# Performance work log

Measured on AMD Instinct MI355X. Metric: run time of the kernel, lower is better.

## Reference

```python
import jax, jax.numpy as jnp
import numpy as np

N = 50000
E = 800000
IN_CH = 128
HID = 32
HEADS = 8
OUT_CH = 64
NEG_SLOPE = 0.2  # PyG GATConv default leaky_relu slope


def setup_inputs() -> dict:
    key = jax.random.key(0)
    ks = jax.random.split(key, 16)
    x = jax.random.normal(ks[0], (N, IN_CH), dtype=jnp.float32)
    edge_index = jax.random.randint(ks[1], (2, E), 0, N, dtype=jnp.int64)
    s = 0.1
    return {
        "x": x,
        "edge_index": edge_index,
        # layer 1: in -> (HEADS, HID), concat
        "W1": jax.random.normal(ks[2], (IN_CH, HEADS * HID), dtype=jnp.float32) * s,
        "att_src1": jax.random.normal(ks[3], (HEADS, HID), dtype=jnp.float32) * s,
        "att_dst1": jax.random.normal(ks[4], (HEADS, HID), dtype=jnp.float32) * s,
        "b1": jnp.zeros((HEADS * HID,), dtype=jnp.float32),
        # layer 2: HEADS*HID -> (HEADS, HID), concat
        "W2": jax.random.normal(ks[5], (HEADS * HID, HEADS * HID), dtype=jnp.float32) * s,
        "att_src2": jax.random.normal(ks[6], (HEADS, HID), dtype=jnp.float32) * s,
        "att_dst2": jax.random.normal(ks[7], (HEADS, HID), dtype=jnp.float32) * s,
        "b2": jnp.zeros((HEADS * HID,), dtype=jnp.float32),
        # layer 3: HEADS*HID -> (1, OUT_CH), no concat (heads=1)
        "W3": jax.random.normal(ks[8], (HEADS * HID, OUT_CH), dtype=jnp.float32) * s,
        "att_src3": jax.random.normal(ks[9], (1, OUT_CH), dtype=jnp.float32) * s,
        "att_dst3": jax.random.normal(ks[10], (1, OUT_CH), dtype=jnp.float32) * s,
        "b3": jnp.zeros((OUT_CH,), dtype=jnp.float32),
    }


def gat_conv(x, src, dst, W, a_src, a_dst, b, heads, ch, concat):
    n = x.shape[0]
    h = (x @ W).reshape(n, heads, ch)                      # [N,H,C]
    alpha_src = jnp.sum(h * a_src, axis=-1)                # [N,H]
    alpha_dst = jnp.sum(h * a_dst, axis=-1)                # [N,H]
    logits = jax.nn.leaky_relu(alpha_src[src] + alpha_dst[dst], NEG_SLOPE)  # [E,H]
    # numerically stable softmax over edges grouped by destination node
    m = jax.ops.segment_max(logits, dst, num_segments=n)   # [N,H]
    m = jnp.where(jnp.isfinite(m), m, 0.0)
    e = jnp.exp(logits - m[dst])                           # [E,H]
    denom = jax.ops.segment_sum(e, dst, num_segments=n)    # [N,H]
    alpha = e / (denom[dst] + 1e-16)                       # [E,H]
    # weighted scatter-aggregate of source features
    out = jax.ops.segment_sum(alpha[:, :, None] * h[src], dst, num_segments=n)  # [N,H,C]
    out = out.reshape(n, heads * ch) if concat else out.mean(axis=1)
    return out + b


def reference(x, edge_index, W1, att_src1, att_dst1, b1,
              W2, att_src2, att_dst2, b2, W3, att_src3, att_dst3, b3):
    src, dst = edge_index[0], edge_index[1]
    h = jax.nn.elu(gat_conv(x, src, dst, W1, att_src1, att_dst1, b1, HEADS, HID, True))
    h = jax.nn.elu(gat_conv(h, src, dst, W2, att_src2, att_dst2, b2, HEADS, HID, True))
    out = gat_conv(h, src, dst, W3, att_src3, att_dst3, b3, 1, OUT_CH, False)
    return out
```

## Files before the change

kernel.cpp:

```cpp
#include <hip/hip_runtime.h>
#include <hip/hip_bf16.h>
#include <hip/hip_fp16.h>
#include <stdint.h>

#define NNODES 50000
#define NEDGES 800000

typedef float f32x4 __attribute__((ext_vector_type(4)));
typedef _Float16 half8 __attribute__((ext_vector_type(8)));

__device__ __forceinline__ ushort f2h(float f) {
  return __half_as_ushort(__float2half(f));
}
__device__ __forceinline__ float2 h2x2(uint32_t u) {
  return __half22float2(__builtin_bit_cast(__half2, u));
}

__device__ __forceinline__ void gload_lds16(const void* g, void* l) {
  __builtin_amdgcn_global_load_lds(
      (const __attribute__((address_space(1))) uint32_t*)g,
      (__attribute__((address_space(3))) uint32_t*)l, 16, 0, 0);
}

__global__ __launch_bounds__(256) void gemm_wide(
    const ushort* __restrict__ A, const ushort* __restrict__ B,
    const float* __restrict__ a_src, const float* __restrict__ a_dst,
    float* __restrict__ as_out, float* __restrict__ ad_out,
    ushort* __restrict__ Cout, int M, int K) {
  __shared__ ushort As[64 * 64];
  __shared__ ushort Bs[256 * 64];

  const int t = threadIdx.x;
  const int w = t >> 6, ln = t & 63;
  const int row0 = blockIdx.x * 64;
  const int wr = (w >> 1) * 32, wc = (w & 1) * 128;

  f32x4 acc[2][8] = {};

  const int nkt = K >> 6;
  for (int kt = 0; kt < nkt; ++kt) {
    const int k0 = kt << 6;
    #pragma unroll
    for (int i = 0; i < 2; ++i) {
      int row8 = w * 2 + i;
      int rloc = row8 * 8 + (ln >> 3);
      int slot = (ln & 7) ^ (rloc & 7);
      int grow = row0 + rloc; grow = grow < M ? grow : M - 1;
      gload_lds16(A + (size_t)grow * K + k0 + slot * 8, As + row8 * 512);
    }
    #pragma unroll
    for (int i = 0; i < 8; ++i) {
      int row8 = w * 8 + i;
      int rloc = row8 * 8 + (ln >> 3);
      int slot = (ln & 7) ^ (rloc & 7);
      gload_lds16(B + (size_t)rloc * K + k0 + slot * 8, Bs + row8 * 512);
    }
    __syncthreads();

    #pragma unroll
    for (int ks = 0; ks < 2; ++ks) {
      half8 a[2], b[8];
      #pragma unroll
      for (int i = 0; i < 2; ++i) {
        int row = wr + i * 16 + (ln & 15);
        int slot = (ks * 4 + (ln >> 4)) ^ (row & 7);
        a[i] = *(const half8*)(As + row * 64 + slot * 8);
      }
      #pragma unroll
      for (int j = 0; j < 8; ++j) {
        int col = wc + j * 16 + (ln & 15);
        int slot = (ks * 4 + (ln >> 4)) ^ (col & 7);
        b[j] = *(const half8*)(Bs + col * 64 + slot * 8);
      }
      #pragma unroll
      for (int i = 0; i < 2; ++i)
        #pragma unroll
        for (int j = 0; j < 8; ++j)
          acc[i][j] = __builtin_amdgcn_mfma_f32_16x16x32_f16(a[i], b[j], acc[i][j], 0, 0, 0);
    }
    __syncthreads();
  }

  const int lx = ln & 15, g = ln >> 4;

  #pragma unroll
  for (int i = 0; i < 2; ++i)
    #pragma unroll
    for (int j = 0; j < 8; ++j)
      #pragma unroll
      for (int r = 0; r < 4; ++r) {
        int grow = row0 + wr + i * 16 + g * 4 + r;
        int gcol = wc + j * 16 + lx;
        if (grow < M) Cout[(size_t)grow * 256 + gcol] = f2h(acc[i][j][r]);
      }

  const int hbase = wc >> 5;
  float avs[8], avd[8];
  #pragma unroll
  for (int j = 0; j < 8; ++j) {
    avs[j] = a_src[wc + j * 16 + lx];
    avd[j] = a_dst[wc + j * 16 + lx];
  }
  #pragma unroll
  for (int i = 0; i < 2; ++i)
    #pragma unroll
    for (int r = 0; r < 4; ++r) {
      float ps[4] = {0.f, 0.f, 0.f, 0.f}, pd[4] = {0.f, 0.f, 0.f, 0.f};
      #pragma unroll
      for (int j = 0; j < 8; ++j) {
        float v = acc[i][j][r];
        ps[j >> 1] += v * avs[j];
        pd[j >> 1] += v * avd[j];
      }
      #pragma unroll
      for (int m = 1; m < 16; m <<= 1)
        #pragma unroll
        for (int q = 0; q < 4; ++q) {
          ps[q] += __shfl_xor(ps[q], m);
          pd[q] += __shfl_xor(pd[q], m);
        }
      if (lx == 0) {
        int grow = row0 + wr + i * 16 + g * 4 + r;
        if (grow < M) {
          #pragma unroll
          for (int q = 0; q < 4; ++q) {
            as_out[grow * 8 + hbase + q] = ps[q];
            ad_out[grow * 8 + hbase + q] = pd[q];
          }
        }
      }
    }
}

__global__ __launch_bounds__(256) void gemm_mfma3(
    const ushort* __restrict__ A, const ushort* __restrict__ B,
    const float* __restrict__ a_src, const float* __restrict__ a_dst,
    float* __restrict__ as_out, float* __restrict__ ad_out,
    ushort* __restrict__ Cout, int M, int K, int Ncols) {
  __shared__ ushort As[128 * 64];
  __shared__ ushort Bs[64 * 64];
  __shared__ float redS[2][128], redD[2][128];

  const int t = threadIdx.x;
  const int w = t >> 6, ln = t & 63;
  const int row0 = blockIdx.y * 128;
  const int col0 = blockIdx.x * 64;
  const int wr = (w >> 1) * 64, wc = (w & 1) * 32;

  f32x4 acc[4][2] = {};

  const int nkt = K >> 6;
  for (int kt = 0; kt < nkt; ++kt) {
    const int k0 = kt << 6;
    #pragma unroll
    for (int i = 0; i < 4; ++i) {
      int row8 = w * 4 + i;
      int rloc = row8 * 8 + (ln >> 3);
      int slot = (ln & 7) ^ (rloc & 7);
      int grow = row0 + rloc; grow = grow < M ? grow : M - 1;
      gload_lds16(A + (size_t)grow * K + k0 + slot * 8, As + row8 * 512);
    }
    #pragma unroll
    for (int i = 0; i < 2; ++i) {
      int row8 = w * 2 + i;
      int rloc = row8 * 8 + (ln >> 3);
      int slot = (ln & 7) ^ (rloc & 7);
      gload_lds16(B + (size_t)(col0 + rloc) * K + k0 + slot * 8, Bs + row8 * 512);
    }
    __syncthreads();

    #pragma unroll
    for (int ks = 0; ks < 2; ++ks) {
      half8 a[4], b[2];
      #pragma unroll
      for (int i = 0; i < 4; ++i) {
        int row = wr + i * 16 + (ln & 15);
        int slot = (ks * 4 + (ln >> 4)) ^ (row & 7);
        a[i] = *(const half8*)(As + row * 64 + slot * 8);
      }
      #pragma unroll
      for (int j = 0; j < 2; ++j) {
        int col = wc + j * 16 + (ln & 15);
        int slot = (ks * 4 + (ln >> 4)) ^ (col & 7);
        b[j] = *(const half8*)(Bs + col * 64 + slot * 8);
      }
      #pragma unroll
      for (int i = 0; i < 4; ++i)
        #pragma unroll
        for (int j = 0; j < 2; ++j)
          acc[i][j] = __builtin_amdgcn_mfma_f32_16x16x32_f16(a[i], b[j], acc[i][j], 0, 0, 0);
    }
    __syncthreads();
  }

  const int lx = ln & 15, g = ln >> 4;

  #pragma unroll
  for (int i = 0; i < 4; ++i)
    #pragma unroll
    for (int j = 0; j < 2; ++j)
      #pragma unroll
      for (int r = 0; r < 4; ++r) {
        int grow = row0 + wr + i * 16 + g * 4 + r;
        int gcol = col0 + wc + j * 16 + lx;
        if (grow < M) Cout[(size_t)grow * Ncols + gcol] = f2h(acc[i][j][r]);
      }

  float avs[2], avd[2];
  #pragma unroll
  for (int j = 0; j < 2; ++j) {
    avs[j] = a_src[wc + j * 16 + lx];
    avd[j] = a_dst[wc + j * 16 + lx];
  }
  #pragma unroll
  for (int i = 0; i < 4; ++i)
    #pragma unroll
    for (int r = 0; r < 4; ++r) {
      float ps = 0.f, pd = 0.f;
      #pragma unroll
      for (int j = 0; j < 2; ++j) {
        float v = acc[i][j][r];
        ps += v * avs[j];
        pd += v * avd[j];
      }
      #pragma unroll
      for (int m = 1; m < 16; m <<= 1) {
        ps += __shfl_xor(ps, m);
        pd += __shfl_xor(pd, m);
      }
      if (lx == 0) {
        int lrow = wr + i * 16 + g * 4 + r;
        redS[w & 1][lrow] = ps;
        redD[w & 1][lrow] = pd;
      }
    }
  __syncthreads();
  if (t < 128) {
    int grow = row0 + t;
    if (grow < M) {
      as_out[grow] = redS[0][t] + redS[1][t];
      ad_out[grow] = redD[0][t] + redD[1][t];
    }
  }
}

__global__ void cvt_h(const float* __restrict__ in, ushort* __restrict__ out, int n4) {
  int idx = blockIdx.x * blockDim.x + threadIdx.x;
  if (idx >= n4) return;
  float4 v = ((const float4*)in)[idx];
  ushort4 o;
  o.x = f2h(v.x); o.y = f2h(v.y); o.z = f2h(v.z); o.w = f2h(v.w);
  ((ushort4*)out)[idx] = o;
}

__global__ void cvt_w(const float* __restrict__ W, ushort* __restrict__ tr,
                      int K, int N) {
  int idx = blockIdx.x * blockDim.x + threadIdx.x;
  if (idx >= K * N) return;
  int k = idx / N, c = idx - k * N;
  tr[(size_t)c * K + k] = f2h(W[idx]);
}

__global__ void deg_kernel(const int* __restrict__ dst, int* __restrict__ deg, int E) {
  int e = blockIdx.x * blockDim.x + threadIdx.x;
  if (e < E) atomicAdd(&deg[dst[e]], 1);
}

__global__ __launch_bounds__(256) void scan_partial(const int* __restrict__ deg,
                                                    int* __restrict__ rowptr,
                                                    int* __restrict__ blocksum, int n) {
  __shared__ int sdata[256];
  int t = threadIdx.x;
  int base = blockIdx.x * 1024 + t * 4;
  int v[4], s = 0;
  #pragma unroll
  for (int i = 0; i < 4; ++i) {
    v[i] = (base + i < n) ? deg[base + i] : 0;
    s += v[i];
  }
  sdata[t] = s;
  __syncthreads();
  for (int off = 1; off < 256; off <<= 1) {
    int x = (t >= off) ? sdata[t - off] : 0;
    __syncthreads();
    sdata[t] += x;
    __syncthreads();
  }
  int run = sdata[t] - s;
  #pragma unroll
  for (int i = 0; i < 4; ++i) {
    if (base + i < n) rowptr[base + i] = run;
    run += v[i];
  }
  if (t == 255) blocksum[blockIdx.x] = sdata[255];
}

__global__ __launch_bounds__(256) void scan_blocksums(int* __restrict__ blocksum, int nb) {
  __shared__ int sdata[256];
  int t = threadIdx.x;
  int v = (t < nb) ? blocksum[t] : 0;
  sdata[t] = v;
  __syncthreads();
  for (int off = 1; off < 256; off <<= 1) {
    int x = (t >= off) ? sdata[t - off] : 0;
    __syncthreads();
    sdata[t] += x;
    __syncthreads();
  }
  if (t < nb) blocksum[t] = sdata[t] - v;
}

__global__ void scan_add(int* __restrict__ rowptr, const int* __restrict__ blocksum,
                         int* __restrict__ cursor, int n, int E) {
  int idx = blockIdx.x * blockDim.x + threadIdx.x;
  if (idx < n) {
    rowptr[idx] += blocksum[idx >> 10];
    cursor[idx] = 0;
  }
  if (idx == n) rowptr[n] = E;
}

__global__ void scatter_kernel(const int* __restrict__ src, const int* __restrict__ dst,
                               const int* __restrict__ rowptr, int* __restrict__ cursor,
                               int* __restrict__ col_src, int E) {
  int e = blockIdx.x * blockDim.x + threadIdx.x;
  if (e >= E) return;
  int d = dst[e];
  int pos = rowptr[d] + atomicAdd(&cursor[d], 1);
  col_src[pos] = src[e];
}

__global__ __launch_bounds__(256) void aggr_h(
    const int* __restrict__ rowptr, const int* __restrict__ col_src,
    const ushort* __restrict__ h, const float* __restrict__ as_,
    const float* __restrict__ ad_, const float* __restrict__ bias,
    ushort* __restrict__ of, int n) {
  int d = blockIdx.x * 4 + (threadIdx.x >> 6);
  if (d >= n) return;
  int lane = threadIdx.x & 63;
  int c0 = lane * 4;
  int hd = lane >> 3;
  float ad_d = ad_[d * 8 + hd];
  float a0 = 0.f, a1 = 0.f, a2 = 0.f, a3 = 0.f, denom = 0.f;
  int beg = rowptr[d], end = rowptr[d + 1];
  int i = beg;
  for (; i + 2 <= end; i += 2) {
    int s0 = col_src[i], s1 = col_src[i + 1];
    float l0 = as_[s0 * 8 + hd] + ad_d;
    float l1 = as_[s1 * 8 + hd] + ad_d;
    uint2 v0 = *(const uint2*)(h + (size_t)s0 * 256 + c0);
    uint2 v1 = *(const uint2*)(h + (size_t)s1 * 256 + c0);
    l0 = (l0 > 0.f) ? l0 : 0.2f * l0;
    l1 = (l1 > 0.f) ? l1 : 0.2f * l1;
    float e0 = __expf(l0), e1 = __expf(l1);
    denom += e0 + e1;
    float2 p0 = h2x2(v0.x), p1 = h2x2(v0.y);
    float2 q0 = h2x2(v1.x), q1 = h2x2(v1.y);
    a0 += e0 * p0.x + e1 * q0.x;
    a1 += e0 * p0.y + e1 * q0.y;
    a2 += e0 * p1.x + e1 * q1.x;
    a3 += e0 * p1.y + e1 * q1.y;
  }
  if (i < end) {
    int s = col_src[i];
    float l = as_[s * 8 + hd] + ad_d;
    l = (l > 0.f) ? l : 0.2f * l;
    float ev = __expf(l);
    denom += ev;
    uint2 v = *(const uint2*)(h + (size_t)s * 256 + c0);
    float2 p0 = h2x2(v.x), p1 = h2x2(v.y);
    a0 += ev * p0.x;
    a1 += ev * p0.y;
    a2 += ev * p1.x;
    a3 += ev * p1.y;
  }
  float inv = 1.f / (denom + 1e-16f);
  float v0 = a0 * inv + bias[c0 + 0];
  float v1 = a1 * inv + bias[c0 + 1];
  float v2 = a2 * inv + bias[c0 + 2];
  float v3 = a3 * inv + bias[c0 + 3];
  v0 = (v0 > 0.f) ? v0 : expm1f(v0);
  v1 = (v1 > 0.f) ? v1 : expm1f(v1);
  v2 = (v2 > 0.f) ? v2 : expm1f(v2);
  v3 = (v3 > 0.f) ? v3 : expm1f(v3);
  ushort4 hh;
  hh.x = f2h(v0); hh.y = f2h(v1); hh.z = f2h(v2); hh.w = f2h(v3);
  *(ushort4*)(of + (size_t)d * 256 + c0) = hh;
}

__global__ __launch_bounds__(256) void aggr_f3(
    const int* __restrict__ rowptr, const int* __restrict__ col_src,
    const ushort* __restrict__ h, const float* __restrict__ as_,
    const float* __restrict__ ad_, const float* __restrict__ bias,
    float* __restrict__ outp, int n) {
  int wid = (blockIdx.x * 256 + threadIdx.x) >> 6;
  int d = wid * 4 + ((threadIdx.x >> 4) & 3);
  if (d >= n) return;
  int l = threadIdx.x & 15;
  int c0 = l * 4;
  float ad_d = ad_[d];
  float a0 = 0.f, a1 = 0.f, a2 = 0.f, a3 = 0.f, denom = 0.f;
  int beg = rowptr[d], end = rowptr[d + 1];
  int i = beg;
  for (; i + 2 <= end; i += 2) {
    int s0 = col_src[i], s1 = col_src[i + 1];
    float l0 = as_[s0] + ad_d;
    float l1 = as_[s1] + ad_d;
    uint2 v0 = *(const uint2*)(h + (size_t)s0 * 64 + c0);
    uint2 v1 = *(const uint2*)(h + (size_t)s1 * 64 + c0);
    l0 = (l0 > 0.f) ? l0 : 0.2f * l0;
    l1 = (l1 > 0.f) ? l1 : 0.2f * l1;
    float e0 = __expf(l0), e1 = __expf(l1);
    denom += e0 + e1;
    float2 p0 = h2x2(v0.x), p1 = h2x2(v0.y);
    float2 q0 = h2x2(v1.x), q1 = h2x2(v1.y);
    a0 += e0 * p0.x + e1 * q0.x;
    a1 += e0 * p0.y + e1 * q0.y;
    a2 += e0 * p1.x + e1 * q1.x;
    a3 += e0 * p1.y + e1 * q1.y;
  }
  if (i < end) {
    int s = col_src[i];
    float lg = as_[s] + ad_d;
    lg = (lg > 0.f) ? lg : 0.2f * lg;
    float ev = __expf(lg);
    denom += ev;
    uint2 v = *(const uint2*)(h + (size_t)s * 64 + c0);
    float2 p0 = h2x2(v.x), p1 = h2x2(v.y);
    a0 += ev * p0.x;
    a1 += ev * p0.y;
    a2 += ev * p1.x;
    a3 += ev * p1.y;
  }
  float inv = 1.f / (denom + 1e-16f);
  float4 r;
  r.x = a0 * inv + bias[c0 + 0];
  r.y = a1 * inv + bias[c0 + 1];
  r.z = a2 * inv + bias[c0 + 2];
  r.w = a3 * inv + bias[c0 + 3];
  *(float4*)(outp + (size_t)d * 64 + c0) = r;
}


extern "C" void kernel_launch(void* const* d_in, const int* in_sizes, int n_in,
                              void* d_out, int out_size, void* d_ws, size_t ws_size,
                              hipStream_t stream) {
  const float* x   = (const float*)d_in[0];
  const int*   ei  = (const int*)d_in[1];
  const float* W1  = (const float*)d_in[2];
  const float* aS1 = (const float*)d_in[3];
  const float* aD1 = (const float*)d_in[4];
  const float* b1  = (const float*)d_in[5];
  const float* W2  = (const float*)d_in[6];
  const float* aS2 = (const float*)d_in[7];
  const float* aD2 = (const float*)d_in[8];
  const float* b2  = (const float*)d_in[9];
  const float* W3  = (const float*)d_in[10];
  const float* aS3 = (const float*)d_in[11];
  const float* aD3 = (const float*)d_in[12];
  const float* b3  = (const float*)d_in[13];

  const int* srcp = ei;
  const int* dstp = ei + NEDGES;

  char* base = (char*)d_ws;
  size_t o = 0;
  ushort* hbf  = (ushort*)(base + o); o += 25600000;
  ushort* ff   = (ushort*)(base + o); o += 25600000;
  ushort* f1   = (ushort*)(base + o); o += 12800000;
  float*  as_  = (float*)(base + o);  o += 1600000;
  float*  ad_  = (float*)(base + o);  o += 1600000;
  ushort* w1t  = (ushort*)(base + o); o += 65536;
  ushort* w2t  = (ushort*)(base + o); o += 131072;
  ushort* w3t  = (ushort*)(base + o); o += 32768;
  int* rowptr  = (int*)(base + o);    o += 200016;
  int* cursor  = (int*)(base + o);    o += 200000;
  int* colsrc  = (int*)(base + o);    o += 3200000;
  int* bsum    = (int*)(base + o);    o += 1024;
  float* outp  = (float*)d_out;

  hipMemsetAsync(cursor, 0, NNODES * sizeof(int), stream);
  deg_kernel<<<(NEDGES + 255) / 256, 256, 0, stream>>>(dstp, cursor, NEDGES);
  int nb = (NNODES + 1023) / 1024;
  scan_partial<<<nb, 256, 0, stream>>>(cursor, rowptr, bsum, NNODES);
  scan_blocksums<<<1, 256, 0, stream>>>(bsum, nb);
  scan_add<<<(NNODES + 256) / 256, 256, 0, stream>>>(rowptr, bsum, cursor, NNODES, NEDGES);
  scatter_kernel<<<(NEDGES + 255) / 256, 256, 0, stream>>>(srcp, dstp, rowptr, cursor,
                                                           colsrc, NEDGES);

  cvt_h<<<(NNODES * 128 / 4 + 255) / 256, 256, 0, stream>>>(x, f1, NNODES * 128 / 4);
  cvt_w<<<(128 * 256 + 255) / 256, 256, 0, stream>>>(W1, w1t, 128, 256);
  cvt_w<<<(256 * 256 + 255) / 256, 256, 0, stream>>>(W2, w2t, 256, 256);
  cvt_w<<<(256 * 64 + 255) / 256, 256, 0, stream>>>(W3, w3t, 256, 64);

  const int ga  = (NNODES + 3) / 4;
  const int ga4 = (NNODES + 15) / 16;
  const int gw  = (NNODES + 63) / 64;
  gemm_wide<<<gw, 256, 0, stream>>>(f1, w1t, aS1, aD1, as_, ad_, hbf, NNODES, 128);
  aggr_h<<<ga, 256, 0, stream>>>(rowptr, colsrc, hbf, as_, ad_, b1, ff, NNODES);
  gemm_wide<<<gw, 256, 0, stream>>>(ff, w2t, aS2, aD2, as_, ad_, hbf, NNODES, 256);
  aggr_h<<<ga, 256, 0, stream>>>(rowptr, colsrc, hbf, as_, ad_, b2, ff, NNODES);
  gemm_mfma3<<<dim3(1, (NNODES + 127) / 128), 256, 0, stream>>>(
      ff, w3t, aS3, aD3, as_, ad_, hbf, NNODES, 256, 64);
  aggr_f3<<<ga4, 256, 0, stream>>>(rowptr, colsrc, hbf, as_, ad_, b3, outp, NNODES);
}
```

Before: 345.4 us.

## Use packed fp16 dot2 and exp2 with prescaled logits in edge aggregation

New measurement: 330.5 us. 4.3% less time.

```diff
diff --git a/kernel.cpp b/kernel.cpp
--- a/kernel.cpp
+++ b/kernel.cpp
@@ -5,15 +5,35 @@
 
 #define NNODES 50000
 #define NEDGES 800000
+#define LOG2E 1.44269504088896340736f
 
 typedef float f32x4 __attribute__((ext_vector_type(4)));
 typedef _Float16 half8 __attribute__((ext_vector_type(8)));
+typedef _Float16 half2v __attribute__((ext_vector_type(2)));
 
 __device__ __forceinline__ ushort f2h(float f) {
   return __half_as_ushort(__float2half(f));
 }
 __device__ __forceinline__ float2 h2x2(uint32_t u) {
   return __half22float2(__builtin_bit_cast(__half2, u));
+}
+
+#if __has_builtin(__builtin_amdgcn_fdot2) && __has_builtin(__builtin_amdgcn_perm) && __has_builtin(__builtin_amdgcn_cvt_pkrtz)
+#define USE_DOT2 1
+#else
+#define USE_DOT2 0
+#endif
+
+__device__ __forceinline__ half2v pack2(float a, float b) {
+  return __builtin_bit_cast(half2v, __builtin_amdgcn_cvt_pkrtz(a, b));
+}
+
+__device__ __forceinline__ float fexp2(float x) {
+#if __has_builtin(__builtin_amdgcn_exp2f)
+  return __builtin_amdgcn_exp2f(x);
+#else
+  return exp2f(x);
+#endif
 }
 
 __device__ __forceinline__ void gload_lds16(const void* g, void* l) {
@@ -98,8 +118,8 @@
   float avs[8], avd[8];
   #pragma unroll
   for (int j = 0; j < 8; ++j) {
-    avs[j] = a_src[wc + j * 16 + lx];
-    avd[j] = a_dst[wc + j * 16 + lx];
+    avs[j] = a_src[wc + j * 16 + lx] * LOG2E;
+    avd[j] = a_dst[wc + j * 16 + lx] * LOG2E;
   }
   #pragma unroll
   for (int i = 0; i < 2; ++i)
@@ -209,8 +229,8 @@
   float avs[2], avd[2];
   #pragma unroll
   for (int j = 0; j < 2; ++j) {
-    avs[j] = a_src[wc + j * 16 + lx];
-    avd[j] = a_dst[wc + j * 16 + lx];
+    avs[j] = a_src[wc + j * 16 + lx] * LOG2E;
+    avd[j] = a_dst[wc + j * 16 + lx] * LOG2E;
   }
   #pragma unroll
   for (int i = 0; i < 4; ++i)
@@ -342,32 +362,54 @@
   int hd = lane >> 3;
   float ad_d = ad_[d * 8 + hd];
   float a0 = 0.f, a1 = 0.f, a2 = 0.f, a3 = 0.f, denom = 0.f;
+  const ushort* hp = h + c0;
   int beg = rowptr[d], end = rowptr[d + 1];
   int i = beg;
-  for (; i + 2 <= end; i += 2) {
-    int s0 = col_src[i], s1 = col_src[i + 1];
+#if USE_DOT2
+  const half2v onepk = {(_Float16)1.f, (_Float16)1.f};
+  for (; i + 4 <= end; i += 4) {
+    int s0 = col_src[i], s1 = col_src[i + 1], s2 = col_src[i + 2], s3 = col_src[i + 3];
     float l0 = as_[s0 * 8 + hd] + ad_d;
     float l1 = as_[s1 * 8 + hd] + ad_d;
-    uint2 v0 = *(const uint2*)(h + (size_t)s0 * 256 + c0);
-    uint2 v1 = *(const uint2*)(h + (size_t)s1 * 256 + c0);
-    l0 = (l0 > 0.f) ? l0 : 0.2f * l0;
-    l1 = (l1 > 0.f) ? l1 : 0.2f * l1;
-    float e0 = __expf(l0), e1 = __expf(l1);
-    denom += e0 + e1;
-    float2 p0 = h2x2(v0.x), p1 = h2x2(v0.y);
-    float2 q0 = h2x2(v1.x), q1 = h2x2(v1.y);
-    a0 += e0 * p0.x + e1 * q0.x;
-    a1 += e0 * p0.y + e1 * q0.y;
-    a2 += e0 * p1.x + e1 * q1.x;
-    a3 += e0 * p1.y + e1 * q1.y;
-  }
-  if (i < end) {
+    float l2 = as_[s2 * 8 + hd] + ad_d;
+    float l3 = as_[s3 * 8 + hd] + ad_d;
+    uint2 v0 = *(const uint2*)(hp + (size_t)s0 * 256);
+    uint2 v1 = *(const uint2*)(hp + (size_t)s1 * 256);
+    uint2 v2 = *(const uint2*)(hp + (size_t)s2 * 256);
+    uint2 v3 = *(const uint2*)(hp + (size_t)s3 * 256);
+    float e0 = fexp2(fmaxf(l0, 0.2f * l0));
+    float e1 = fexp2(fmaxf(l1, 0.2f * l1));
+    float e2 = fexp2(fmaxf(l2, 0.2f * l2));
+    float e3 = fexp2(fmaxf(l3, 0.2f * l3));
+    half2v ep01 = pack2(e0, e1);
+    half2v ep23 = pack2(e2, e3);
+    denom = __builtin_amdgcn_fdot2(ep01, onepk, denom, false);
+    denom = __builtin_amdgcn_fdot2(ep23, onepk, denom, false);
+    uint32_t p;
+    p = __builtin_amdgcn_perm(v1.x, v0.x, 0x05040100u);
+    a0 = __builtin_amdgcn_fdot2(ep01, __builtin_bit_cast(half2v, p), a0, false);
+    p = __builtin_amdgcn_perm(v1.x, v0.x, 0x07060302u);
+    a1 = __builtin_amdgcn_fdot2(ep01, __builtin_bit_cast(half2v, p), a1, false);
+    p = __builtin_amdgcn_perm(v1.y, v0.y, 0x05040100u);
+    a2 = __builtin_amdgcn_fdot2(ep01, __builtin_bit_cast(half2v, p), a2, false);
+    p = __builtin_amdgcn_perm(v1.y, v0.y, 0x07060302u);
+    a3 = __builtin_amdgcn_fdot2(ep01, __builtin_bit_cast(half2v, p), a3, false);
+    p = __builtin_amdgcn_perm(v3.x, v2.x, 0x05040100u);
+    a0 = __builtin_amdgcn_fdot2(ep23, __builtin_bit_cast(half2v, p), a0, false);
+    p = __builtin_amdgcn_perm(v3.x, v2.x, 0x07060302u);
+    a1 = __builtin_amdgcn_fdot2(ep23, __builtin_bit_cast(half2v, p), a1, false);
+    p = __builtin_amdgcn_perm(v3.y, v2.y, 0x05040100u);
+    a2 = __builtin_amdgcn_fdot2(ep23, __builtin_bit_cast(half2v, p), a2, false);
+    p = __builtin_amdgcn_perm(v3.y, v2.y, 0x07060302u);
+    a3 = __builtin_amdgcn_fdot2(ep23, __builtin_bit_cast(half2v, p), a3, false);
+  }
+#endif
+  for (; i < end; ++i) {
     int s = col_src[i];
     float l = as_[s * 8 + hd] + ad_d;
-    l = (l > 0.f) ? l : 0.2f * l;
-    float ev = __expf(l);
+    float ev = fexp2(fmaxf(l, 0.2f * l));
     denom += ev;
-    uint2 v = *(const uint2*)(h + (size_t)s * 256 + c0);
+    uint2 v = *(const uint2*)(hp + (size_t)s * 256);
     float2 p0 = h2x2(v.x), p1 = h2x2(v.y);
     a0 += ev * p0.x;
     a1 += ev * p0.y;
@@ -400,32 +442,38 @@
   int c0 = l * 4;
   float ad_d = ad_[d];
   float a0 = 0.f, a1 = 0.f, a2 = 0.f, a3 = 0.f, denom = 0.f;
+  const ushort* hp = h + c0;
   int beg = rowptr[d], end = rowptr[d + 1];
   int i = beg;
+#if USE_DOT2
+  const half2v onepk = {(_Float16)1.f, (_Float16)1.f};
   for (; i + 2 <= end; i += 2) {
     int s0 = col_src[i], s1 = col_src[i + 1];
     float l0 = as_[s0] + ad_d;
     float l1 = as_[s1] + ad_d;
-    uint2 v0 = *(const uint2*)(h + (size_t)s0 * 64 + c0);
-    uint2 v1 = *(const uint2*)(h + (size_t)s1 * 64 + c0);
-    l0 = (l0 > 0.f) ? l0 : 0.2f * l0;
-    l1 = (l1 > 0.f) ? l1 : 0.2f * l1;
-    float e0 = __expf(l0), e1 = __expf(l1);
-    denom += e0 + e1;
-    float2 p0 = h2x2(v0.x), p1 = h2x2(v0.y);
-    float2 q0 = h2x2(v1.x), q1 = h2x2(v1.y);
-    a0 += e0 * p0.x + e1 * q0.x;
-    a1 += e0 * p0.y + e1 * q0.y;
-    a2 += e0 * p1.x + e1 * q1.x;
-    a3 += e0 * p1.y + e1 * q1.y;
-  }
-  if (i < end) {
+    uint2 v0 = *(const uint2*)(hp + (size_t)s0 * 64);
+    uint2 v1 = *(const uint2*)(hp + (size_t)s1 * 64);
+    float e0 = fexp2(fmaxf(l0, 0.2f * l0));
+    float e1 = fexp2(fmaxf(l1, 0.2f * l1));
+    half2v ep = pack2(e0, e1);
+    denom = __builtin_amdgcn_fdot2(ep, onepk, denom, false);
+    uint32_t p;
+    p = __builtin_amdgcn_perm(v1.x, v0.x, 0x05040100u);
+    a0 = __builtin_amdgcn_fdot2(ep, __builtin_bit_cast(half2v, p), a0, false);
+    p = __builtin_amdgcn_perm(v1.x, v0.x, 0x07060302u);
+    a1 = __builtin_amdgcn_fdot2(ep, __builtin_bit_cast(half2v, p), a1, false);
+    p = __builtin_amdgcn_perm(v1.y, v0.y, 0x05040100u);
+    a2 = __builtin_amdgcn_fdot2(ep, __builtin_bit_cast(half2v, p), a2, false);
+    p = __builtin_amdgcn_perm(v1.y, v0.y, 0x07060302u);
+    a3 = __builtin_amdgcn_fdot2(ep, __builtin_bit_cast(half2v, p), a3, false);
+  }
+#endif
+  for (; i < end; ++i) {
     int s = col_src[i];
     float lg = as_[s] + ad_d;
-    lg = (lg > 0.f) ? lg : 0.2f * lg;
-    float ev = __expf(lg);
+    float ev = fexp2(fmaxf(lg, 0.2f * lg));
     denom += ev;
-    uint2 v = *(const uint2*)(h + (size_t)s * 64 + c0);
+    uint2 v = *(const uint2*)(hp + (size_t)s * 64);
     float2 p0 = h2x2(v.x), p1 = h2x2(v.y);
     a0 += ev * p0.x;
     a1 += ev * p0.y;
```
